# Kernel optimization log

Measured on AMD Instinct MI355X. Metric: run time of the kernel, lower is better.

## Reference

```python
import jax, jax.numpy as jnp
import numpy as np

N_X, N_U, N_Y, HID, T = 1024, 512, 128, 4096, 8192


def setup_inputs() -> dict:
    key = jax.random.key(0)
    ks = jax.random.split(key, 6)
    s = lambda fan_in: 1.0 / np.sqrt(fan_in)
    return {
        "x0": jax.random.normal(ks[0], (N_X,), jnp.float32),
        "u": jax.random.normal(ks[1], (T, N_U), jnp.float32),
        "f_w1": jax.random.normal(ks[2], (N_X + N_U, HID), jnp.float32) * s(N_X + N_U),
        "f_b1": jnp.zeros((HID,), jnp.float32),
        "f_w2": jax.random.normal(ks[3], (HID, N_X), jnp.float32) * s(HID),
        "f_b2": jnp.zeros((N_X,), jnp.float32),
        "g_w1": jax.random.normal(ks[4], (N_X, HID), jnp.float32) * s(N_X),
        "g_b1": jnp.zeros((HID,), jnp.float32),
        "g_w2": jax.random.normal(ks[5], (HID, N_Y), jnp.float32) * s(HID),
        "g_b2": jnp.zeros((N_Y,), jnp.float32),
    }


def reference(x0, u, f_w1, f_b1, f_w2, f_b2, g_w1, g_b1, g_w2, g_b2):
    # Simulator: scan over time; each step:
    #   xu = concat(x, u_t); new_x = f_xu(xu); y_t = g_x(x)
    def step(x, u_t):
        xu = jnp.concatenate([x, u_t])                       # [n_x + n_u]
        new_x = jnp.tanh(xu @ f_w1 + f_b1) @ f_w2 + f_b2     # [n_x]
        y_t = jnp.tanh(x @ g_w1 + g_b1) @ g_w2 + g_b2        # [n_y]
        return new_x, y_t

    _, y = jax.lax.scan(step, x0, u)                         # y: [T, n_y]
    return y
```

## Files before the change

kernel.cpp:

```cpp
#include <hip/hip_runtime.h>
#include <hip/hip_bf16.h>
#include <stdint.h>

#define T_STEPS 8192
#define NX 1024
#define NU 512
#define NY 128
#define HID 4096

#define SEQ_WGS 256
#define SEQ_BLK 512

typedef __attribute__((ext_vector_type(8))) short bf16x8;
typedef __attribute__((ext_vector_type(4))) float f32x4;
typedef __attribute__((ext_vector_type(2))) short s16x2;

__device__ __forceinline__ float bf2f(ushort u) {
  union { uint32_t i; float f; } v; v.i = ((uint32_t)u) << 16; return v.f;
}
__device__ __forceinline__ ushort f2bf(float f) {
  union { float f; uint32_t i; } v; v.f = f;
  uint32_t r = v.i + 0x7fffu + ((v.i >> 16) & 1u);
  return (ushort)(r >> 16);
}
__device__ __forceinline__ float lof(uint32_t u) {
  union { uint32_t i; float f; } v; v.i = u << 16; return v.f;
}
__device__ __forceinline__ float hif(uint32_t u) {
  union { uint32_t i; float f; } v; v.i = u & 0xffff0000u; return v.f;
}

__device__ __forceinline__ float dot2bf(uint32_t h, uint32_t m, float acc) {
#if __has_builtin(__builtin_amdgcn_fdot2_f32_bf16)
  return __builtin_amdgcn_fdot2_f32_bf16(__builtin_bit_cast(s16x2, h),
                                         __builtin_bit_cast(s16x2, m), acc, false);
#else
  acc = fmaf(lof(h), lof(m), acc);
  return fmaf(hif(h), hif(m), acc);
#endif
}


__global__ void cvt_bf16_kernel(const float* __restrict__ in, ushort* __restrict__ out, int n) {
  int i = blockIdx.x * blockDim.x + threadIdx.x;
  int stride = gridDim.x * blockDim.x;
  for (; i < n; i += stride) out[i] = f2bf(in[i]);
}

__global__ void transpose_cvt_kernel(const float* __restrict__ in, ushort* __restrict__ out,
                                     int R, int C) {
  __shared__ float tile[32][33];
  int bx = blockIdx.x, by = blockIdx.y;
  int tx = threadIdx.x, ty = threadIdx.y;
#pragma unroll
  for (int yy = 0; yy < 4; ++yy) {
    long r = (long)by * 32 + ty + yy * 8;
    long c = (long)bx * 32 + tx;
    tile[ty + yy * 8][tx] = in[r * C + c];
  }
  __syncthreads();
#pragma unroll
  for (int yy = 0; yy < 4; ++yy) {
    long c = (long)bx * 32 + ty + yy * 8;
    long r = (long)by * 32 + tx;
    out[c * R + r] = f2bf(tile[tx][ty + yy * 8]);
  }
}

__global__ void bias_dh_kernel(const float* __restrict__ fw1, const float* __restrict__ fb1,
                               const float* __restrict__ fb2, float* __restrict__ biasDH) {
  int j = blockIdx.x * blockDim.x + threadIdx.x;
  float s = fb1[j];
  for (int k = 0; k < NX; ++k) s += fb2[k] * fw1[(long)k * HID + j];
  biasDH[j] = s;
}

__global__ void fixup_row0_kernel(const float* __restrict__ fw1, const float* __restrict__ fb1,
                                  const float* __restrict__ u, const float* __restrict__ x0,
                                  ushort* __restrict__ DH, uint32_t* __restrict__ htag) {
  int j = blockIdx.x * blockDim.x + threadIdx.x;
  float s = fb1[j];
  for (int k = 0; k < NU; ++k) s += u[k] * fw1[(long)(NX + k) * HID + j];
  for (int k = 0; k < NX; ++k) s += x0[k] * fw1[(long)k * HID + j];
  float h = tanhf(s);
  ushort hb = f2bf(h);
  DH[j] = hb;
  htag[j] = ((uint32_t)hb << 16);
}

__global__ void x0_row_kernel(const float* __restrict__ x0, ushort* __restrict__ X) {
  int j = blockIdx.x * blockDim.x + threadIdx.x;
  if (j < NX) X[j] = f2bf(x0[j]);
}

#define GBM 128
#define GBN 128
#define GBK 32
#define LDT 40

__global__ __launch_bounds__(256) void gemm_kernel(
    const ushort* __restrict__ A, const ushort* __restrict__ BT,
    void* __restrict__ Cout, const float* __restrict__ bias,
    int M, int N, int K, int flags)
{
  __shared__ ushort Al[GBM * LDT];
  __shared__ ushort Bl[GBN * LDT];
  const int tid = threadIdx.x;
  const int bm = blockIdx.y, bn = blockIdx.x;
  const int wave = tid >> 6, lane = tid & 63;
  const int wr = wave >> 1, wc = wave & 1;
  const int l15 = lane & 15, l4 = lane >> 4;

  f32x4 acc[4][4];
#pragma unroll
  for (int m = 0; m < 4; ++m)
#pragma unroll
    for (int n = 0; n < 4; ++n) acc[m][n] = (f32x4){0.f, 0.f, 0.f, 0.f};

  const int r_t = tid >> 1;
  const int h_t = (tid & 1) * 16;
  const long arow = (long)bm * GBM + r_t;
  const long brow = (long)bn * GBN + r_t;

  for (int k0 = 0; k0 < K; k0 += GBK) {
    uint4 a0 = make_uint4(0,0,0,0), a1 = make_uint4(0,0,0,0);
    if (arow < M) {
      const ushort* p = A + arow * K + k0 + h_t;
      a0 = *(const uint4*)p;
      a1 = *(const uint4*)(p + 8);
    }
    const ushort* q = BT + brow * K + k0 + h_t;
    uint4 b0 = *(const uint4*)q;
    uint4 b1 = *(const uint4*)(q + 8);
    __syncthreads();
    *(uint4*)&Al[r_t * LDT + h_t]     = a0;
    *(uint4*)&Al[r_t * LDT + h_t + 8] = a1;
    *(uint4*)&Bl[r_t * LDT + h_t]     = b0;
    *(uint4*)&Bl[r_t * LDT + h_t + 8] = b1;
    __syncthreads();

    bf16x8 af[4], bfv[4];
#pragma unroll
    for (int m = 0; m < 4; ++m)
      af[m] = *(const bf16x8*)&Al[(wr * 64 + m * 16 + l15) * LDT + l4 * 8];
#pragma unroll
    for (int n = 0; n < 4; ++n)
      bfv[n] = *(const bf16x8*)&Bl[(wc * 64 + n * 16 + l15) * LDT + l4 * 8];
#pragma unroll
    for (int m = 0; m < 4; ++m)
#pragma unroll
      for (int n = 0; n < 4; ++n)
        acc[m][n] = __builtin_amdgcn_mfma_f32_16x16x32_bf16(af[m], bfv[n], acc[m][n], 0, 0, 0);
  }

  const bool f32out = (flags & 2) != 0;
  const bool dotanh = (flags & 1) != 0;
#pragma unroll
  for (int m = 0; m < 4; ++m) {
#pragma unroll
    for (int n = 0; n < 4; ++n) {
#pragma unroll
      for (int j = 0; j < 4; ++j) {
        long grow = (long)bm * GBM + wr * 64 + m * 16 + l4 * 4 + j;
        int  gcol = bn * GBN + wc * 64 + n * 16 + l15;
        if (grow < M) {
          float v = acc[m][n][j];
          if (bias) v += bias[gcol];
          if (dotanh) v = tanhf(v);
          if (f32out) ((float*)Cout)[grow * N + gcol] = v;
          else        ((ushort*)Cout)[grow * N + gcol] = f2bf(v);
        }
      }
    }
  }
}

__global__ __launch_bounds__(SEQ_BLK, 1) void seq_kernel(
    const ushort* __restrict__ MT, ushort* __restrict__ DH,
    uint32_t* __restrict__ htag, int nsteps)
{
  __shared__ ushort hl[HID];
  const int tid = threadIdx.x;
  const int w = threadIdx.x >> 6;
  const int lane = tid & 63;
  const int c0 = (blockIdx.x << 4) + (w << 1);

  uint4 mA[8], mB[8];
  {
    const uint4* rA = (const uint4*)(MT + (size_t)c0 * HID);
    const uint4* rB = (const uint4*)(MT + (size_t)(c0 + 1) * HID);
#pragma unroll
    for (int j = 0; j < 8; ++j) {
      mA[j] = rA[lane + 64 * j];
      mB[j] = rB[lane + 64 * j];
    }
  }

  const bool prod = (lane == 0);
  unsigned long long* tagbase = (unsigned long long*)htag;

  for (int i = 0; i < nsteps; ++i) {
    float dA = 0.f, dB = 0.f;
    if (prod) {
      uint32_t dw = *(const uint32_t*)(DH + (size_t)(i + 1) * HID + c0);
      dA = lof(dw); dB = hif(dw);
    }

    unsigned long long x0, x1, x2, x3;
    {
      unsigned long long* slot = tagbase + (size_t)(i & 1) * (HID / 2) + (tid << 2);
      const uint32_t tg = (uint32_t)i & 0xffffu;
      for (;;) {
        x0 = __hip_atomic_load(slot + 0, __ATOMIC_RELAXED, __HIP_MEMORY_SCOPE_AGENT);
        x1 = __hip_atomic_load(slot + 1, __ATOMIC_RELAXED, __HIP_MEMORY_SCOPE_AGENT);
        x2 = __hip_atomic_load(slot + 2, __ATOMIC_RELAXED, __HIP_MEMORY_SCOPE_AGENT);
        x3 = __hip_atomic_load(slot + 3, __ATOMIC_RELAXED, __HIP_MEMORY_SCOPE_AGENT);
        uint32_t bad = (((uint32_t)x0 ^ tg) | ((uint32_t)x1 ^ tg) |
                        ((uint32_t)x2 ^ tg) | ((uint32_t)x3 ^ tg)) & 0xffffu;
        if (bad == 0) break;
        __builtin_amdgcn_s_sleep(1);
      }
    }
    __syncthreads();
    {
      uint4 p;
      p.x = ((uint32_t)(x0 >> 16) & 0xffffu) | ((uint32_t)(x0 >> 32) & 0xffff0000u);
      p.y = ((uint32_t)(x1 >> 16) & 0xffffu) | ((uint32_t)(x1 >> 32) & 0xffff0000u);
      p.z = ((uint32_t)(x2 >> 16) & 0xffffu) | ((uint32_t)(x2 >> 32) & 0xffff0000u);
      p.w = ((uint32_t)(x3 >> 16) & 0xffffu) | ((uint32_t)(x3 >> 32) & 0xffff0000u);
      ((uint4*)hl)[tid] = p;
    }
    __syncthreads();

    float accA = 0.f, accB = 0.f;
    const uint4* h4 = (const uint4*)hl;
#pragma unroll
    for (int j = 0; j < 8; ++j) {
      uint4 hv = h4[lane + 64 * j];
      accA = dot2bf(hv.x, mA[j].x, accA);
      accB = dot2bf(hv.x, mB[j].x, accB);
      accA = dot2bf(hv.y, mA[j].y, accA);
      accB = dot2bf(hv.y, mB[j].y, accB);
      accA = dot2bf(hv.z, mA[j].z, accA);
      accB = dot2bf(hv.z, mB[j].z, accB);
      accA = dot2bf(hv.w, mA[j].w, accA);
      accB = dot2bf(hv.w, mB[j].w, accB);
    }
#pragma unroll
    for (int off = 32; off >= 1; off >>= 1) {
      accA += __shfl_xor(accA, off, 64);
      accB += __shfl_xor(accB, off, 64);
    }

    if (prod) {
      ushort ha = f2bf(tanhf(accA + dA));
      ushort hb = f2bf(tanhf(accB + dB));
      uint32_t tg1 = (uint32_t)(i + 1) & 0xffffu;
      unsigned long long word =
          ((unsigned long long)(((uint32_t)hb << 16) | tg1) << 32) |
          (unsigned long long)(((uint32_t)ha << 16) | tg1);
      __hip_atomic_store(tagbase + (size_t)((i + 1) & 1) * (HID / 2) + (c0 >> 1), word,
                         __ATOMIC_RELAXED, __HIP_MEMORY_SCOPE_AGENT);
      *(uint32_t*)(DH + (size_t)(i + 1) * HID + c0) = (uint32_t)ha | ((uint32_t)hb << 16);
    }
  }
}


extern "C" void kernel_launch(void* const* d_in, const int* in_sizes, int n_in,
                              void* d_out, int out_size, void* d_ws, size_t ws_size,
                              hipStream_t stream) {
  const float* x0  = (const float*)d_in[0];
  const float* u   = (const float*)d_in[1];
  const float* fw1 = (const float*)d_in[2];
  const float* fb1 = (const float*)d_in[3];
  const float* fw2 = (const float*)d_in[4];
  const float* fb2 = (const float*)d_in[5];
  const float* gw1 = (const float*)d_in[6];
  const float* gb1 = (const float*)d_in[7];
  const float* gw2 = (const float*)d_in[8];
  const float* gb2 = (const float*)d_in[9];
  float* out = (float*)d_out;

  char* ws = (char*)d_ws;
  size_t off = 0;
  auto alloc = [&](size_t bytes) -> char* {
    char* p = ws + off; off += (bytes + 255) & ~(size_t)255; return p;
  };
  ushort* MT     = (ushort*)alloc((size_t)HID * HID * 2);
  ushort* DH     = (ushort*)alloc((size_t)T_STEPS * HID * 2);
  ushort* X      = (ushort*)alloc((size_t)T_STEPS * NX * 2);
  ushort* W1xT   = (ushort*)alloc((size_t)HID * NX * 2);
  ushort* W1uT   = (ushort*)alloc((size_t)HID * NU * 2);
  ushort* W2bf   = (ushort*)alloc((size_t)HID * NX * 2);
  ushort* W2T    = (ushort*)alloc((size_t)NX * HID * 2);
  ushort* Gw1T   = (ushort*)alloc((size_t)HID * NX * 2);
  ushort* Gw2T   = (ushort*)alloc((size_t)NY * HID * 2);
  ushort* Ubf    = (ushort*)alloc((size_t)T_STEPS * NU * 2);
  float*  biasDH = (float*)alloc((size_t)HID * 4);
  uint32_t* htag = (uint32_t*)alloc((size_t)2 * HID * 4);
  if (off > ws_size) return;

  cvt_bf16_kernel<<<2048, 256, 0, stream>>>(u, Ubf, T_STEPS * NU);
  cvt_bf16_kernel<<<2048, 256, 0, stream>>>(fw2, W2bf, HID * NX);
  transpose_cvt_kernel<<<dim3(HID/32, NX/32), dim3(32, 8), 0, stream>>>(fw1, W1xT, NX, HID);
  transpose_cvt_kernel<<<dim3(HID/32, NU/32), dim3(32, 8), 0, stream>>>(fw1 + (size_t)NX * HID, W1uT, NU, HID);
  transpose_cvt_kernel<<<dim3(NX/32, HID/32), dim3(32, 8), 0, stream>>>(fw2, W2T, HID, NX);
  transpose_cvt_kernel<<<dim3(HID/32, NX/32), dim3(32, 8), 0, stream>>>(gw1, Gw1T, NX, HID);
  transpose_cvt_kernel<<<dim3(NY/32, HID/32), dim3(32, 8), 0, stream>>>(gw2, Gw2T, HID, NY);
  bias_dh_kernel<<<HID/256, 256, 0, stream>>>(fw1, fb1, fb2, biasDH);

  gemm_kernel<<<dim3(HID/128, HID/128), 256, 0, stream>>>(W1xT, W2bf, MT, nullptr, HID, HID, NX, 0);
  gemm_kernel<<<dim3(HID/128, T_STEPS/128), 256, 0, stream>>>(Ubf, W1uT, DH, biasDH, T_STEPS, HID, NU, 0);
  fixup_row0_kernel<<<HID/256, 256, 0, stream>>>(fw1, fb1, u, x0, DH, htag);

  {
    int nsteps = T_STEPS - 2;
    void* MT_p = (void*)MT; void* DH_p = (void*)DH; void* ht_p = (void*)htag;
    void* args[] = { &MT_p, &DH_p, &ht_p, &nsteps };
    hipError_t e = hipLaunchCooperativeKernel((const void*)seq_kernel, dim3(SEQ_WGS),
                                              dim3(SEQ_BLK), args, 0, stream);
    if (e != hipSuccess) {
      (void)hipGetLastError();
      seq_kernel<<<SEQ_WGS, SEQ_BLK, 0, stream>>>(MT, DH, htag, nsteps);
    }
  }

  x0_row_kernel<<<NX/256, 256, 0, stream>>>(x0, X);
  gemm_kernel<<<dim3(NX/128, T_STEPS/128), 256, 0, stream>>>(DH, W2T, X + NX, fb2, T_STEPS - 1, NX, HID, 0);
  gemm_kernel<<<dim3(HID/128, T_STEPS/128), 256, 0, stream>>>(X, Gw1T, DH, gb1, T_STEPS, HID, NX, 1);
  gemm_kernel<<<dim3(NY/128, T_STEPS/128), 256, 0, stream>>>(DH, Gw2T, out, gb2, T_STEPS, NY, HID, 2);
}
```

Baseline: 23.35 ms.

## Use a ring of tagged hidden-state rows with per-block sentinel polling

Replaces the double-buffered tagged hidden-state slots with a 128-row ring. Each step, 256 threads poll a single sentinel word per producer block and then all threads do plain vector loads of the row, re-spinning only on words whose tag is stale. The cross-lane reduction is also merged so both outputs share one shuffle tree. The aim is to cut the cost of the per-step global spin, which previously had every thread atomically polling four words. The ring trades workspace for fewer overwrite hazards, and the plain loads rely on per-word tags for correctness.

After: 18.93 ms. 1.23x faster.

```diff
diff --git a/kernel.cpp b/kernel.cpp
--- a/kernel.cpp
+++ b/kernel.cpp
@@ -10,6 +10,7 @@
 
 #define SEQ_WGS 256
 #define SEQ_BLK 512
+#define RING 128
 
 typedef __attribute__((ext_vector_type(8))) short bf16x8;
 typedef __attribute__((ext_vector_type(4))) float f32x4;
@@ -40,6 +41,11 @@
 #endif
 }
 
+__device__ __forceinline__ void fixw(uint32_t& x, uint32_t* wp, uint32_t tg) {
+  while ((x & 0xffffu) != tg)
+    x = __hip_atomic_load(wp, __ATOMIC_RELAXED, __HIP_MEMORY_SCOPE_AGENT);
+}
+
 
 __global__ void cvt_bf16_kernel(const float* __restrict__ in, ushort* __restrict__ out, int n) {
   int i = blockIdx.x * blockDim.x + threadIdx.x;
@@ -77,7 +83,7 @@
 
 __global__ void fixup_row0_kernel(const float* __restrict__ fw1, const float* __restrict__ fb1,
                                   const float* __restrict__ u, const float* __restrict__ x0,
-                                  ushort* __restrict__ DH, uint32_t* __restrict__ htag) {
+                                  ushort* __restrict__ DH, uint32_t* __restrict__ HTAG) {
   int j = blockIdx.x * blockDim.x + threadIdx.x;
   float s = fb1[j];
   for (int k = 0; k < NU; ++k) s += u[k] * fw1[(long)(NX + k) * HID + j];
@@ -85,7 +91,7 @@
   float h = tanhf(s);
   ushort hb = f2bf(h);
   DH[j] = hb;
-  htag[j] = ((uint32_t)hb << 16);
+  HTAG[j] = ((uint32_t)hb << 16);
 }
 
 __global__ void x0_row_kernel(const float* __restrict__ x0, ushort* __restrict__ X) {
@@ -177,11 +183,11 @@
 
 __global__ __launch_bounds__(SEQ_BLK, 1) void seq_kernel(
     const ushort* __restrict__ MT, ushort* __restrict__ DH,
-    uint32_t* __restrict__ htag, int nsteps)
+    uint32_t* __restrict__ HTAG, int nsteps)
 {
   __shared__ ushort hl[HID];
   const int tid = threadIdx.x;
-  const int w = threadIdx.x >> 6;
+  const int w = tid >> 6;
   const int lane = tid & 63;
   const int c0 = (blockIdx.x << 4) + (w << 1);
 
@@ -197,38 +203,48 @@
   }
 
   const bool prod = (lane == 0);
-  unsigned long long* tagbase = (unsigned long long*)htag;
 
   for (int i = 0; i < nsteps; ++i) {
+    const uint32_t tg = (uint32_t)i & 0xffffu;
+    uint32_t* rowp = HTAG + (size_t)(i & (RING - 1)) * HID;
+
     float dA = 0.f, dB = 0.f;
     if (prod) {
       uint32_t dw = *(const uint32_t*)(DH + (size_t)(i + 1) * HID + c0);
       dA = lof(dw); dB = hif(dw);
     }
 
-    unsigned long long x0, x1, x2, x3;
+    if (tid < SEQ_WGS) {
+      uint32_t* sp = rowp + tid * 16 + 15;
+      while ((__hip_atomic_load(sp, __ATOMIC_RELAXED, __HIP_MEMORY_SCOPE_AGENT)
+              & 0xffffu) != tg)
+        __builtin_amdgcn_s_sleep(1);
+    }
+    __syncthreads();
+
     {
-      unsigned long long* slot = tagbase + (size_t)(i & 1) * (HID / 2) + (tid << 2);
-      const uint32_t tg = (uint32_t)i & 0xffffu;
-      for (;;) {
-        x0 = __hip_atomic_load(slot + 0, __ATOMIC_RELAXED, __HIP_MEMORY_SCOPE_AGENT);
-        x1 = __hip_atomic_load(slot + 1, __ATOMIC_RELAXED, __HIP_MEMORY_SCOPE_AGENT);
-        x2 = __hip_atomic_load(slot + 2, __ATOMIC_RELAXED, __HIP_MEMORY_SCOPE_AGENT);
-        x3 = __hip_atomic_load(slot + 3, __ATOMIC_RELAXED, __HIP_MEMORY_SCOPE_AGENT);
-        uint32_t bad = (((uint32_t)x0 ^ tg) | ((uint32_t)x1 ^ tg) |
-                        ((uint32_t)x2 ^ tg) | ((uint32_t)x3 ^ tg)) & 0xffffu;
-        if (bad == 0) break;
-        __builtin_amdgcn_s_sleep(1);
+      const uint4* rv = (const uint4*)rowp;
+      uint4 v0 = rv[tid];
+      uint4 v1 = rv[tid + 512];
+      uint32_t bad0 = ((v0.x ^ tg) | (v0.y ^ tg) | (v0.z ^ tg) | (v0.w ^ tg)) & 0xffffu;
+      if (__builtin_expect(bad0 != 0, 0)) {
+        uint32_t* wp = rowp + tid * 4;
+        fixw(v0.x, wp + 0, tg); fixw(v0.y, wp + 1, tg);
+        fixw(v0.z, wp + 2, tg); fixw(v0.w, wp + 3, tg);
       }
-    }
-    __syncthreads();
-    {
-      uint4 p;
-      p.x = ((uint32_t)(x0 >> 16) & 0xffffu) | ((uint32_t)(x0 >> 32) & 0xffff0000u);
-      p.y = ((uint32_t)(x1 >> 16) & 0xffffu) | ((uint32_t)(x1 >> 32) & 0xffff0000u);
-      p.z = ((uint32_t)(x2 >> 16) & 0xffffu) | ((uint32_t)(x2 >> 32) & 0xffff0000u);
-      p.w = ((uint32_t)(x3 >> 16) & 0xffffu) | ((uint32_t)(x3 >> 32) & 0xffff0000u);
-      ((uint4*)hl)[tid] = p;
+      uint32_t bad1 = ((v1.x ^ tg) | (v1.y ^ tg) | (v1.z ^ tg) | (v1.w ^ tg)) & 0xffffu;
+      if (__builtin_expect(bad1 != 0, 0)) {
+        uint32_t* wp = rowp + tid * 4 + 2048;
+        fixw(v1.x, wp + 0, tg); fixw(v1.y, wp + 1, tg);
+        fixw(v1.z, wp + 2, tg); fixw(v1.w, wp + 3, tg);
+      }
+      unsigned long long* hl64 = (unsigned long long*)hl;
+      uint32_t p0 = (v0.x >> 16) | (v0.y & 0xffff0000u);
+      uint32_t p1 = (v0.z >> 16) | (v0.w & 0xffff0000u);
+      hl64[tid] = ((unsigned long long)p1 << 32) | p0;
+      p0 = (v1.x >> 16) | (v1.y & 0xffff0000u);
+      p1 = (v1.z >> 16) | (v1.w & 0xffff0000u);
+      hl64[tid + 512] = ((unsigned long long)p1 << 32) | p0;
     }
     __syncthreads();
 
@@ -246,21 +262,24 @@
       accA = dot2bf(hv.w, mA[j].w, accA);
       accB = dot2bf(hv.w, mB[j].w, accB);
     }
-#pragma unroll
-    for (int off = 32; off >= 1; off >>= 1) {
-      accA += __shfl_xor(accA, off, 64);
-      accB += __shfl_xor(accB, off, 64);
-    }
+    accA += __shfl_xor(accA, 32, 64);
+    accB += __shfl_xor(accB, 32, 64);
+    float y = (lane < 32) ? accA : accB;
+#pragma unroll
+    for (int off = 16; off >= 1; off >>= 1)
+      y += __shfl_xor(y, off, 64);
+    float totB = __shfl(y, 32, 64);
 
     if (prod) {
-      ushort ha = f2bf(tanhf(accA + dA));
-      ushort hb = f2bf(tanhf(accB + dB));
+      ushort ha = f2bf(tanhf(y + dA));
+      ushort hb = f2bf(tanhf(totB + dB));
       uint32_t tg1 = (uint32_t)(i + 1) & 0xffffu;
       unsigned long long word =
           ((unsigned long long)(((uint32_t)hb << 16) | tg1) << 32) |
           (unsigned long long)(((uint32_t)ha << 16) | tg1);
-      __hip_atomic_store(tagbase + (size_t)((i + 1) & 1) * (HID / 2) + (c0 >> 1), word,
-                         __ATOMIC_RELAXED, __HIP_MEMORY_SCOPE_AGENT);
+      unsigned long long* dst =
+          (unsigned long long*)(HTAG + (size_t)((i + 1) & (RING - 1)) * HID) + (c0 >> 1);
+      __hip_atomic_store(dst, word, __ATOMIC_RELAXED, __HIP_MEMORY_SCOPE_AGENT);
       *(uint32_t*)(DH + (size_t)(i + 1) * HID + c0) = (uint32_t)ha | ((uint32_t)hb << 16);
     }
   }
@@ -298,7 +317,7 @@
   ushort* Gw2T   = (ushort*)alloc((size_t)NY * HID * 2);
   ushort* Ubf    = (ushort*)alloc((size_t)T_STEPS * NU * 2);
   float*  biasDH = (float*)alloc((size_t)HID * 4);
-  uint32_t* htag = (uint32_t*)alloc((size_t)2 * HID * 4);
+  uint32_t* HTAG = (uint32_t*)alloc((size_t)RING * HID * 4);
   if (off > ws_size) return;
 
   cvt_bf16_kernel<<<2048, 256, 0, stream>>>(u, Ubf, T_STEPS * NU);
@@ -312,17 +331,17 @@
 
   gemm_kernel<<<dim3(HID/128, HID/128), 256, 0, stream>>>(W1xT, W2bf, MT, nullptr, HID, HID, NX, 0);
   gemm_kernel<<<dim3(HID/128, T_STEPS/128), 256, 0, stream>>>(Ubf, W1uT, DH, biasDH, T_STEPS, HID, NU, 0);
-  fixup_row0_kernel<<<HID/256, 256, 0, stream>>>(fw1, fb1, u, x0, DH, htag);
+  fixup_row0_kernel<<<HID/256, 256, 0, stream>>>(fw1, fb1, u, x0, DH, HTAG);
 
   {
     int nsteps = T_STEPS - 2;
-    void* MT_p = (void*)MT; void* DH_p = (void*)DH; void* ht_p = (void*)htag;
+    void* MT_p = (void*)MT; void* DH_p = (void*)DH; void* ht_p = (void*)HTAG;
     void* args[] = { &MT_p, &DH_p, &ht_p, &nsteps };
     hipError_t e = hipLaunchCooperativeKernel((const void*)seq_kernel, dim3(SEQ_WGS),
                                               dim3(SEQ_BLK), args, 0, stream);
     if (e != hipSuccess) {
       (void)hipGetLastError();
-      seq_kernel<<<SEQ_WGS, SEQ_BLK, 0, stream>>>(MT, DH, htag, nsteps);
+      seq_kernel<<<SEQ_WGS, SEQ_BLK, 0, stream>>>(MT, DH, HTAG, nsteps);
     }
   }
 
```
